# Performance work log

Hardware: AMD Instinct MI355X
Metric: run time of the kernel (lower is better)

The kernel has to match this reference:

```python
import jax, jax.numpy as jnp
import numpy as np

B, T, H, L = 16384, 100, 32, 6  # batch voxels, time frames, hidden, layers


def setup_inputs() -> dict:
    key = jax.random.key(0)
    ks = jax.random.split(key, 12)
    s = 0.1  # small init scale akin to PyTorch's uniform(-1/sqrt(H), 1/sqrt(H))
    F = L * H  # 192, head input dim
    return {
        "x": jax.random.normal(ks[0], (B, T, 1), jnp.float32),
        "W_ih0": jax.random.normal(ks[1], (3 * H, 1), jnp.float32) * s,   # layer 0 input weights
        "W_ih": jax.random.normal(ks[2], (L - 1, 3 * H, H), jnp.float32) * s,  # layers 1..5
        "W_hh": jax.random.normal(ks[3], (L, 3 * H, H), jnp.float32) * s,
        "b_ih": jax.random.normal(ks[4], (L, 3 * H), jnp.float32) * s,
        "b_hh": jax.random.normal(ks[5], (L, 3 * H), jnp.float32) * s,
        "Wk": jax.random.normal(ks[6], (1, F), jnp.float32) * s,
        "bk": jax.random.normal(ks[7], (1,), jnp.float32) * s,
        "We": jax.random.normal(ks[8], (1, F), jnp.float32) * s,
        "be": jax.random.normal(ks[9], (1,), jnp.float32) * s,
        "Wt": jax.random.normal(ks[10], (1, F), jnp.float32) * s,
        "bt": jax.random.normal(ks[11], (1,), jnp.float32) * s,
    }


def _gru_layer(x_seq, Wi, Wh, bi, bh):
    # x_seq: [T, B, D_in]; gate order (r, z, n) matches torch.nn.GRU
    xw = jnp.einsum('tbd,gd->tbg', x_seq, Wi) + bi  # precompute input projections [T,B,3H]

    def step(h, xw_t):
        hg = h @ Wh.T + bh                      # [B, 3H]
        xr, xz, xn = jnp.split(xw_t, 3, axis=-1)
        hr, hz, hn = jnp.split(hg, 3, axis=-1)
        r = jax.nn.sigmoid(xr + hr)
        z = jax.nn.sigmoid(xz + hz)
        n = jnp.tanh(xn + r * hn)
        h_new = (1.0 - z) * n + z * h
        return h_new, h_new

    h0 = jnp.zeros((x_seq.shape[1], Wh.shape[1]), x_seq.dtype)
    h_last, out = jax.lax.scan(step, h0, xw)
    return out, h_last


def reference(x, W_ih0, W_ih, W_hh, b_ih, b_hh, Wk, bk, We, be, Wt, bt):
    seq = jnp.transpose(x, (1, 0, 2))  # [T, B, 1] (time-major for scan)
    finals = []
    seq, h_last = _gru_layer(seq, W_ih0, W_hh[0], b_ih[0], b_hh[0])
    finals.append(h_last)
    for l in range(1, L):
        seq, h_last = _gru_layer(seq, W_ih[l - 1], W_hh[l], b_ih[l], b_hh[l])
        finals.append(h_last)
    # rearrange 'l n h -> n (l h)'
    feat = jnp.transpose(jnp.stack(finals), (1, 0, 2)).reshape(x.shape[0], L * H)
    ktrans = feat @ Wk.T + bk
    kep = feat @ We.T + be
    t0 = feat @ Wt.T + bt
    return (ktrans, kep, t0)
```

## Files before the change

kernel.cpp:

```cpp
#include <hip/hip_runtime.h>

#define T_LEN 100
#define H 32
#define L 6
#define NT 6
#define TPB 512
#define BT 32
#define NPAIR 25
#define NK (NPAIR + L - 1)
#define S1 1.44269504088896f

typedef float f32x4  __attribute__((ext_vector_type(4)));
typedef _Float16 f16x8 __attribute__((ext_vector_type(8)));

union FragU { f16x8 h; f32x4 f; unsigned int u[4]; };

__device__ inline unsigned short f2h(float f) {
    union { _Float16 h; unsigned short u; } v; v.h = (_Float16)f; return v.u;
}
__device__ inline float rcpa(float x)  { return __builtin_amdgcn_rcpf(x); }
__device__ inline float exp2b(float x) { return __builtin_amdgcn_exp2f(x); }

__device__ inline unsigned int pk16(float a, float b) {
    unsigned int h;
    asm("v_cvt_pkrtz_f16_f32 %0, %1, %2" : "=v"(h) : "v"(a), "v"(b));
    return h;
}

__global__ void pack_frags(const float* __restrict__ Whh, const float* __restrict__ Wih,
                           unsigned short* __restrict__ WhFhi,
                           unsigned short* __restrict__ WiFhi)
{
    int tid = blockIdx.x * blockDim.x + threadIdx.x;
    const int NWH = L * NT * 64;
    const int NWI = (L - 1) * NT * 64;
    if (tid >= NWH + NWI) return;
    const float* src; unsigned short *dhi; int tile, lane;
    if (tid < NWH) {
        int l = tid / (NT * 64); int r = tid % (NT * 64); tile = r / 64; lane = r % 64;
        src = Whh + l * 96 * H;
        dhi = WhFhi + tid * 8;
    } else {
        int t2 = tid - NWH;
        int l = t2 / (NT * 64); int r = t2 % (NT * 64); tile = r / 64; lane = r % 64;
        src = Wih + l * 96 * H;
        dhi = WiFhi + t2 * 8;
    }
    int row = tile * 16 + (lane & 15);
    int gk  = lane >> 4;
    float scale = (row < 64) ? -S1 : -2.0f * S1;
    unsigned short thi[8];
#pragma unroll
    for (int e = 0; e < 8; ++e) {
        int j = ((e >> 2) << 4) + (gk << 2) + (e & 3);
        thi[e] = f2h(scale * src[row * H + j]);
    }
    *(uint4*)dhi = *(const uint4*)thi;
}

__global__ __launch_bounds__(TPB, 2) void gru_mfma(
    const float* __restrict__ x,
    const float* __restrict__ Wih0,
    const float* __restrict__ bih,
    const float* __restrict__ bhh,
    const unsigned short* __restrict__ WhFhi,
    const unsigned short* __restrict__ WiFhi,
    const float* __restrict__ Wk, const float* __restrict__ bk,
    const float* __restrict__ We, const float* __restrict__ be,
    const float* __restrict__ Wt, const float* __restrict__ bt,
    float* __restrict__ out, int B)
{
    __shared__ unsigned char slot[5][2][4][2048];
    __shared__ float xt[T_LEN][BT];
    __shared__ float hpart[L][3][BT];

    const int tid  = threadIdx.x;
    const int wv   = tid >> 6;
    const int lane = tid & 63;
    const int b    = lane & 15;
    const int g    = lane >> 4;
    const int b0   = blockIdx.x * BT;

    int layer, grmask;
    switch (wv) {
      case 0: layer = 0; grmask = 3; break;
      case 4: layer = 1; grmask = 1; break;
      case 1: layer = 2; grmask = 3; break;
      case 5: layer = 1; grmask = 2; break;
      case 2: layer = 3; grmask = 3; break;
      case 6: layer = 5; grmask = 1; break;
      case 3: layer = 4; grmask = 3; break;
      default: layer = 5; grmask = 2; break;
    }

    for (int idx = tid; idx < T_LEN * BT; idx += TPB) {
        int bb = idx / T_LEN, t = idx % T_LEN;
        xt[t][bb] = x[(b0 + bb) * T_LEN + t];
    }

    f16x8 whh[NT], wih[NT];
#pragma unroll
    for (int t6 = 0; t6 < NT; ++t6)
        whh[t6] = ((const f16x8*)WhFhi)[(layer * NT + t6) * 64 + lane];
    if (layer > 0) {
#pragma unroll
        for (int t6 = 0; t6 < NT; ++t6)
            wih[t6] = ((const f16x8*)WiFhi)[((layer - 1) * NT + t6) * 64 + lane];
    }

    f32x4 bc[4], bxn[2], bhn[2];
    {
        const int rb = g * 4;
#pragma unroll
        for (int t6 = 0; t6 < 4; ++t6)
#pragma unroll
            for (int r = 0; r < 4; ++r) {
                int row = t6 * 16 + rb + r;
                bc[t6][r] = -S1 * (bih[layer * 96 + row] + bhh[layer * 96 + row]);
            }
#pragma unroll
        for (int tt = 0; tt < 2; ++tt)
#pragma unroll
            for (int r = 0; r < 4; ++r) {
                int row = 64 + tt * 16 + rb + r;
                bxn[tt][r] = -2.0f * S1 * bih[layer * 96 + row];
                bhn[tt][r] = -2.0f * S1 * bhh[layer * 96 + row];
            }
        if (layer == 0) {
#pragma unroll
            for (int t6 = 0; t6 < NT; ++t6) {
                FragU u;
#pragma unroll
                for (int r = 0; r < 4; ++r) {
                    int row = t6 * 16 + rb + r;
                    float s = (row < 64) ? -S1 : -2.0f * S1;
                    u.f[r] = s * Wih0[row];
                }
                wih[t6] = u.h;
            }
        }
    }

    float hp[2][8];
#pragma unroll
    for (int gr = 0; gr < 2; ++gr)
#pragma unroll
        for (int i = 0; i < 8; ++i) hp[gr][i] = 0.0f;
    f16x8 hfH[2] = {{0,0,0,0,0,0,0,0},{0,0,0,0,0,0,0,0}};

    const int soff = b * 64 + ((g ^ ((b >> 1) & 3)) << 4);
    unsigned char* const sbase = (unsigned char*)slot;

    auto do_step2 = [&](int t, int rq, int wp, int st) {
        f32x4 acc[2][4], accX[2][2], accH[2][2];
        f16x8 iH[2];
        if (layer > 0) {
            const unsigned char* ru = sbase + (((layer - 1) * 8 + rq * 4 + st) << 11);
            if (grmask & 1) iH[0] = *(const f16x8*)(ru + soff);
            if (grmask & 2) iH[1] = *(const f16x8*)(ru + 1024 + soff);
        }
        __builtin_amdgcn_s_setprio(1);
#pragma unroll
        for (int gr = 0; gr < 2; ++gr)
            if (grmask & (1 << gr)) {
#pragma unroll
                for (int t6 = 0; t6 < 4; ++t6)
                    acc[gr][t6] = __builtin_amdgcn_mfma_f32_16x16x32_f16(whh[t6], hfH[gr], bc[t6], 0, 0, 0);
#pragma unroll
                for (int tt = 0; tt < 2; ++tt)
                    accH[gr][tt] = __builtin_amdgcn_mfma_f32_16x16x32_f16(whh[4 + tt], hfH[gr], bhn[tt], 0, 0, 0);
            }
        if (layer == 0) {
#pragma unroll
            for (int gr = 0; gr < 2; ++gr)
                if (grmask & (1 << gr)) {
                    float xv = xt[t][gr * 16 + b];
#pragma unroll
                    for (int t6 = 0; t6 < 4; ++t6) {
                        FragU u; u.h = wih[t6];
#pragma unroll
                        for (int r = 0; r < 4; ++r)
                            acc[gr][t6][r] = fmaf(u.f[r], xv, acc[gr][t6][r]);
                    }
#pragma unroll
                    for (int tt = 0; tt < 2; ++tt) {
                        FragU u; u.h = wih[4 + tt];
#pragma unroll
                        for (int r = 0; r < 4; ++r)
                            accX[gr][tt][r] = fmaf(u.f[r], xv, bxn[tt][r]);
                    }
                }
        } else {
#pragma unroll
            for (int gr = 0; gr < 2; ++gr)
                if (grmask & (1 << gr)) {
#pragma unroll
                    for (int t6 = 0; t6 < 4; ++t6)
                        acc[gr][t6] = __builtin_amdgcn_mfma_f32_16x16x32_f16(wih[t6], iH[gr], acc[gr][t6], 0, 0, 0);
#pragma unroll
                    for (int tt = 0; tt < 2; ++tt)
                        accX[gr][tt] = __builtin_amdgcn_mfma_f32_16x16x32_f16(wih[4 + tt], iH[gr], bxn[tt], 0, 0, 0);
                }
        }
        __builtin_amdgcn_s_setprio(0);
#pragma unroll
        for (int gr = 0; gr < 2; ++gr)
            if (grmask & (1 << gr)) {
#pragma unroll
                for (int jj = 0; jj < 2; ++jj)
#pragma unroll
                    for (int r = 0; r < 4; ++r) {
                        float Er = exp2b(acc[gr][jj][r]);
                        float Ez = exp2b(acc[gr][2 + jj][r]);
                        float rg = rcpa(1.0f + Er);
                        float u  = fmaf(rg, accH[gr][jj][r], accX[gr][jj][r]);
                        float En = exp2b(u);
                        float en1 = 1.0f + En, ez1 = 1.0f + Ez;
                        float d   = rcpa(en1 * ez1);
                        float t2  = fmaf(-En, Ez, Ez);
                        float num = fmaf(hp[gr][jj * 4 + r], en1, t2);
                        hp[gr][jj * 4 + r] = num * d;
                    }
            }
#pragma unroll
        for (int gr = 0; gr < 2; ++gr)
            if (grmask & (1 << gr)) {
                unsigned int h01 = pk16(hp[gr][0], hp[gr][1]);
                unsigned int h23 = pk16(hp[gr][2], hp[gr][3]);
                unsigned int h45 = pk16(hp[gr][4], hp[gr][5]);
                unsigned int h67 = pk16(hp[gr][6], hp[gr][7]);
                FragU Hu;
                Hu.u[0] = h01; Hu.u[1] = h23; Hu.u[2] = h45; Hu.u[3] = h67;
                hfH[gr] = Hu.h;
                if (layer < L - 1) {
                    unsigned char* wp8 = sbase + ((layer * 8 + wp * 4 + st) << 11) + gr * 1024;
                    *(uint4*)(wp8 + soff) = make_uint4(h01, h23, h45, h67);
                }
            }
    };

    __syncthreads();

    for (int i = 0; i < NK; ++i) {
        int k = i - layer;
        if (0 <= k && k < NPAIR) {
            const int p = i & 1, q = p ^ 1;
#pragma unroll
            for (int st = 0; st < 4; ++st)
                do_step2(4 * k + st, q, p, st);
        }
        __syncthreads();
    }

    {
        const int rb = g * 4;
#pragma unroll
        for (int hd = 0; hd < 3; ++hd) {
            const float* W = (hd == 0) ? Wk : (hd == 1) ? We : Wt;
#pragma unroll
            for (int gr = 0; gr < 2; ++gr)
                if (grmask & (1 << gr)) {
                    float s = 0.0f;
#pragma unroll
                    for (int jj = 0; jj < 2; ++jj)
#pragma unroll
                        for (int r = 0; r < 4; ++r)
                            s = fmaf(W[layer * H + jj * 16 + rb + r], hp[gr][jj * 4 + r], s);
                    s += __shfl_xor(s, 16, 64);
                    s += __shfl_xor(s, 32, 64);
                    if (g == 0) hpart[layer][hd][gr * 16 + b] = s;
                }
        }
        __syncthreads();
        if (wv < 3 && lane < BT) {
            int bb = lane;
            float s = (wv == 0) ? bk[0] : (wv == 1) ? be[0] : bt[0];
#pragma unroll
            for (int l = 0; l < L; ++l) s += hpart[l][wv][bb];
            out[wv * B + b0 + bb] = s;
        }
    }
}

extern "C" void kernel_launch(void* const* d_in, const int* in_sizes, int n_in,
                              void* d_out, int out_size, void* d_ws, size_t ws_size,
                              hipStream_t stream)
{
    const float* x    = (const float*)d_in[0];
    const float* Wih0 = (const float*)d_in[1];
    const float* Wih  = (const float*)d_in[2];
    const float* Whh  = (const float*)d_in[3];
    const float* bih  = (const float*)d_in[4];
    const float* bhh  = (const float*)d_in[5];
    const float* Wk   = (const float*)d_in[6];
    const float* bk   = (const float*)d_in[7];
    const float* We   = (const float*)d_in[8];
    const float* be   = (const float*)d_in[9];
    const float* Wt   = (const float*)d_in[10];
    const float* bt   = (const float*)d_in[11];
    float* out = (float*)d_out;

    const int B = in_sizes[0] / T_LEN;

    unsigned short* WhFhi = (unsigned short*)d_ws;
    unsigned short* WiFhi = WhFhi + L * NT * 64 * 8;

    const int nPack = (L * NT * 64) + ((L - 1) * NT * 64);
    pack_frags<<<(nPack + 255) / 256, 256, 0, stream>>>(Whh, Wih, WhFhi, WiFhi);
    gru_mfma<<<B / BT, TPB, 0, stream>>>(x, Wih0, bih, bhh, WhFhi, WiFhi,
                                         Wk, bk, We, be, Wt, bt, out, B);
}
```

Before: 237.5 us.

## Interleave two batch tiles per block and halve wavefront pipeline chunk

Each block now handles 64 batch elements as two interleaved 32-element tiles, drawn from the first and second halves of the batch. Each wave carries separate hidden-state registers for both tiles and alternates steps between them, so their independent recurrences can overlap MFMA and transcendental latency. The layer-wavefront pipeline now advances two timesteps per barrier instead of four, which shortens the fill/drain bubble but doubles the number of barriers. The costs are more registers per wave, a larger LDS footprint, and half as many blocks, likely leaving one resident block per CU.

```diff
diff --git a/kernel.cpp b/kernel.cpp
--- a/kernel.cpp
+++ b/kernel.cpp
@@ -5,8 +5,8 @@
 #define L 6
 #define NT 6
 #define TPB 512
-#define BT 32
-#define NPAIR 25
+#define BT 64
+#define NPAIR 50
 #define NK (NPAIR + L - 1)
 #define S1 1.44269504088896f
 
@@ -70,7 +70,7 @@
     const float* __restrict__ Wt, const float* __restrict__ bt,
     float* __restrict__ out, int B)
 {
-    __shared__ unsigned char slot[5][2][4][2048];
+    __shared__ unsigned char slot[5][2][2][4096];
     __shared__ float xt[T_LEN][BT];
     __shared__ float hpart[L][3][BT];
 
@@ -79,7 +79,8 @@
     const int lane = tid & 63;
     const int b    = lane & 15;
     const int g    = lane >> 4;
-    const int b0   = blockIdx.x * BT;
+    const int b0   = blockIdx.x * 32;
+    const int HALF = B >> 1;
 
     int layer, grmask;
     switch (wv) {
@@ -95,7 +96,8 @@
 
     for (int idx = tid; idx < T_LEN * BT; idx += TPB) {
         int bb = idx / T_LEN, t = idx % T_LEN;
-        xt[t][bb] = x[(b0 + bb) * T_LEN + t];
+        int batch = (bb < 32) ? (b0 + bb) : (HALF + b0 + bb - 32);
+        xt[t][bb] = x[batch * T_LEN + t];
     }
 
     f16x8 whh[NT], wih[NT];
@@ -141,21 +143,24 @@
         }
     }
 
-    float hp[2][8];
-#pragma unroll
-    for (int gr = 0; gr < 2; ++gr)
-#pragma unroll
-        for (int i = 0; i < 8; ++i) hp[gr][i] = 0.0f;
-    f16x8 hfH[2] = {{0,0,0,0,0,0,0,0},{0,0,0,0,0,0,0,0}};
+    float hp[2][2][8];
+#pragma unroll
+    for (int tl = 0; tl < 2; ++tl)
+#pragma unroll
+        for (int gr = 0; gr < 2; ++gr)
+#pragma unroll
+            for (int i = 0; i < 8; ++i) hp[tl][gr][i] = 0.0f;
+    f16x8 hfH[2][2] = {{{0,0,0,0,0,0,0,0},{0,0,0,0,0,0,0,0}},
+                       {{0,0,0,0,0,0,0,0},{0,0,0,0,0,0,0,0}}};
 
     const int soff = b * 64 + ((g ^ ((b >> 1) & 3)) << 4);
     unsigned char* const sbase = (unsigned char*)slot;
 
-    auto do_step2 = [&](int t, int rq, int wp, int st) {
+    auto do_step2 = [&](int t, int rq, int wp, int st, int tl) {
         f32x4 acc[2][4], accX[2][2], accH[2][2];
         f16x8 iH[2];
         if (layer > 0) {
-            const unsigned char* ru = sbase + (((layer - 1) * 8 + rq * 4 + st) << 11);
+            const unsigned char* ru = sbase + (((layer - 1) * 4 + rq * 2 + st) << 12) + tl * 2048;
             if (grmask & 1) iH[0] = *(const f16x8*)(ru + soff);
             if (grmask & 2) iH[1] = *(const f16x8*)(ru + 1024 + soff);
         }
@@ -165,16 +170,16 @@
             if (grmask & (1 << gr)) {
 #pragma unroll
                 for (int t6 = 0; t6 < 4; ++t6)
-                    acc[gr][t6] = __builtin_amdgcn_mfma_f32_16x16x32_f16(whh[t6], hfH[gr], bc[t6], 0, 0, 0);
+                    acc[gr][t6] = __builtin_amdgcn_mfma_f32_16x16x32_f16(whh[t6], hfH[tl][gr], bc[t6], 0, 0, 0);
 #pragma unroll
                 for (int tt = 0; tt < 2; ++tt)
-                    accH[gr][tt] = __builtin_amdgcn_mfma_f32_16x16x32_f16(whh[4 + tt], hfH[gr], bhn[tt], 0, 0, 0);
+                    accH[gr][tt] = __builtin_amdgcn_mfma_f32_16x16x32_f16(whh[4 + tt], hfH[tl][gr], bhn[tt], 0, 0, 0);
             }
         if (layer == 0) {
 #pragma unroll
             for (int gr = 0; gr < 2; ++gr)
                 if (grmask & (1 << gr)) {
-                    float xv = xt[t][gr * 16 + b];
+                    float xv = xt[t][tl * 32 + gr * 16 + b];
 #pragma unroll
                     for (int t6 = 0; t6 < 4; ++t6) {
                         FragU u; u.h = wih[t6];
@@ -218,22 +223,22 @@
                         float en1 = 1.0f + En, ez1 = 1.0f + Ez;
                         float d   = rcpa(en1 * ez1);
                         float t2  = fmaf(-En, Ez, Ez);
-                        float num = fmaf(hp[gr][jj * 4 + r], en1, t2);
-                        hp[gr][jj * 4 + r] = num * d;
+                        float num = fmaf(hp[tl][gr][jj * 4 + r], en1, t2);
+                        hp[tl][gr][jj * 4 + r] = num * d;
                     }
             }
 #pragma unroll
         for (int gr = 0; gr < 2; ++gr)
             if (grmask & (1 << gr)) {
-                unsigned int h01 = pk16(hp[gr][0], hp[gr][1]);
-                unsigned int h23 = pk16(hp[gr][2], hp[gr][3]);
-                unsigned int h45 = pk16(hp[gr][4], hp[gr][5]);
-                unsigned int h67 = pk16(hp[gr][6], hp[gr][7]);
+                unsigned int h01 = pk16(hp[tl][gr][0], hp[tl][gr][1]);
+                unsigned int h23 = pk16(hp[tl][gr][2], hp[tl][gr][3]);
+                unsigned int h45 = pk16(hp[tl][gr][4], hp[tl][gr][5]);
+                unsigned int h67 = pk16(hp[tl][gr][6], hp[tl][gr][7]);
                 FragU Hu;
                 Hu.u[0] = h01; Hu.u[1] = h23; Hu.u[2] = h45; Hu.u[3] = h67;
-                hfH[gr] = Hu.h;
+                hfH[tl][gr] = Hu.h;
                 if (layer < L - 1) {
-                    unsigned char* wp8 = sbase + ((layer * 8 + wp * 4 + st) << 11) + gr * 1024;
+                    unsigned char* wp8 = sbase + ((layer * 4 + wp * 2 + st) << 12) + tl * 2048 + gr * 1024;
                     *(uint4*)(wp8 + soff) = make_uint4(h01, h23, h45, h67);
                 }
             }
@@ -245,9 +250,10 @@
         int k = i - layer;
         if (0 <= k && k < NPAIR) {
             const int p = i & 1, q = p ^ 1;
-#pragma unroll
-            for (int st = 0; st < 4; ++st)
-                do_step2(4 * k + st, q, p, st);
+            do_step2(2 * k,     q, p, 0, 0);
+            do_step2(2 * k,     q, p, 0, 1);
+            do_step2(2 * k + 1, q, p, 1, 0);
+            do_step2(2 * k + 1, q, p, 1, 1);
         }
         __syncthreads();
     }
@@ -258,26 +264,29 @@
         for (int hd = 0; hd < 3; ++hd) {
             const float* W = (hd == 0) ? Wk : (hd == 1) ? We : Wt;
 #pragma unroll
-            for (int gr = 0; gr < 2; ++gr)
-                if (grmask & (1 << gr)) {
-                    float s = 0.0f;
-#pragma unroll
-                    for (int jj = 0; jj < 2; ++jj)
-#pragma unroll
-                        for (int r = 0; r < 4; ++r)
-                            s = fmaf(W[layer * H + jj * 16 + rb + r], hp[gr][jj * 4 + r], s);
-                    s += __shfl_xor(s, 16, 64);
-                    s += __shfl_xor(s, 32, 64);
-                    if (g == 0) hpart[layer][hd][gr * 16 + b] = s;
-                }
+            for (int tl = 0; tl < 2; ++tl)
+#pragma unroll
+                for (int gr = 0; gr < 2; ++gr)
+                    if (grmask & (1 << gr)) {
+                        float s = 0.0f;
+#pragma unroll
+                        for (int jj = 0; jj < 2; ++jj)
+#pragma unroll
+                            for (int r = 0; r < 4; ++r)
+                                s = fmaf(W[layer * H + jj * 16 + rb + r], hp[tl][gr][jj * 4 + r], s);
+                        s += __shfl_xor(s, 16, 64);
+                        s += __shfl_xor(s, 32, 64);
+                        if (g == 0) hpart[layer][hd][tl * 32 + gr * 16 + b] = s;
+                    }
         }
         __syncthreads();
         if (wv < 3 && lane < BT) {
             int bb = lane;
+            int batch = (bb < 32) ? (b0 + bb) : (HALF + b0 + bb - 32);
             float s = (wv == 0) ? bk[0] : (wv == 1) ? be[0] : bt[0];
 #pragma unroll
             for (int l = 0; l < L; ++l) s += hpart[l][wv][bb];
-            out[wv * B + b0 + bb] = s;
+            out[wv * B + batch] = s;
         }
     }
 }
```

Measured after the change: 236.0 us. Within noise of the previous version (-0.6%).
